# Optimization experiments

Measured on AMD Instinct MI355X. Metric: run time of the kernel, lower is better.

The kernel has to match this reference:

```python
import jax, jax.numpy as jnp
import numpy as np

T, B, D, H = 1024, 64, 512, 512


def setup_inputs() -> dict:
    key = jax.random.key(0)
    ks = jax.random.split(key, 10)
    s_in = 1.0 / np.sqrt(D + H)  # torch Linear default init scale
    inp = {
        "inputs": jax.random.normal(ks[0], (T, B, D), dtype=jnp.float32),
        "Wf": jax.random.uniform(ks[1], (D + H, H), jnp.float32, -s_in, s_in),
        "bf": jax.random.uniform(ks[2], (H,), jnp.float32, -s_in, s_in),
        "Wi": jax.random.uniform(ks[3], (D + H, H), jnp.float32, -s_in, s_in),
        "bi": jax.random.uniform(ks[4], (H,), jnp.float32, -s_in, s_in),
        "Wg": jax.random.uniform(ks[5], (D + H, H), jnp.float32, -s_in, s_in),
        "bg": jax.random.uniform(ks[6], (H,), jnp.float32, -s_in, s_in),
        "Wo": jax.random.uniform(ks[7], (D + H, H), jnp.float32, -s_in, s_in),
        "bo": jax.random.uniform(ks[8], (H,), jnp.float32, -s_in, s_in),
        "phase_bias": jax.random.normal(ks[9], (H,), dtype=jnp.float32) * 0.02,
    }
    return inp


def reference(inputs, Wf, bf, Wi, bi, Wg, bg, Wo, bo, phase_bias):
    gate_scale = 1.0
    Bsz = inputs.shape[1]
    Hd = Wf.shape[1]
    # Fuse the four gate projections into one GEMM per step (same math).
    W = jnp.concatenate([Wf, Wi, Wg, Wo], axis=1)          # [D+H, 4H]
    bias = jnp.concatenate([bf, bi, bg, bo]) * gate_scale + jnp.tile(phase_bias, 4)
    # note: (x@W + b)*s + pb == x@(W*s) + (b*s + pb); gate_scale folded in.
    Ws = W * gate_scale

    h0 = jnp.zeros((Bsz, Hd), dtype=inputs.dtype)
    c0 = jnp.zeros((Bsz, Hd), dtype=inputs.dtype)

    def step(carry, x):
        hx, cx = carry
        combined = jnp.concatenate([x, hx], axis=1)         # [B, D+H]
        z = combined @ Ws + bias                            # [B, 4H]
        zf, zi, zg, zo = jnp.split(z, 4, axis=1)
        f = jax.nn.sigmoid(zf)
        i = jax.nn.sigmoid(zi)
        g = jnp.tanh(zg)
        o = jax.nn.sigmoid(zo)
        cx = f * cx + i * g
        hx = o * jnp.tanh(cx)
        return (hx, cx), hx

    (hx, cx), stacked = jax.lax.scan(step, (h0, c0), inputs)
    return stacked, hx, cx
```

## Files before the change

kernel.cpp:

```cpp
#include <hip/hip_runtime.h>

#define TT 1024
#define BB 64
#define DD 512
#define HH 512
#define NG 4
#define BPG 16
#define NS 32
#define NTHR 256

typedef short s8v __attribute__((ext_vector_type(8)));
typedef float f4v __attribute__((ext_vector_type(4)));
typedef int i4v __attribute__((ext_vector_type(4)));

#define LGKM_BAR()                                          \
  do {                                                      \
    asm volatile("s_waitcnt lgkmcnt(0)" ::: "memory");      \
    __builtin_amdgcn_sched_barrier(0);                      \
    __builtin_amdgcn_s_barrier();                           \
    __builtin_amdgcn_sched_barrier(0);                      \
  } while (0)

static __device__ __forceinline__ unsigned short f2bf(float f) {
  union { float f; unsigned int u; } v; v.f = f;
  unsigned int r = v.u + 0x7FFFu + ((v.u >> 16) & 1u);
  return (unsigned short)(r >> 16);
}
static __device__ __forceinline__ i4v ld_b128_cohere(const void* p) {
  i4v r;
  asm volatile("global_load_dwordx4 %0, %1, off sc0 sc1"
               : "=v"(r) : "v"(p) : "memory");
  return r;
}
static __device__ __forceinline__ int ld_b32_cohere(const void* p) {
  int r;
  asm volatile("global_load_dword %0, %1, off sc0 sc1\n\t"
               "s_waitcnt vmcnt(0)"
               : "=v"(r) : "v"(p) : "memory");
  return r;
}
static __device__ __forceinline__ void st_b32_cohere(void* p, unsigned int v) {
  asm volatile("global_store_dword %0, %1, off sc0 sc1"
               :: "v"(p), "v"(v) : "memory");
}
static __device__ __forceinline__ unsigned int cvtpk_bf16(float lo, float hi) {
  unsigned int r;
  asm("v_cvt_pk_bf16_f32 %0, %1, %2" : "=v"(r) : "v"(lo), "v"(hi));
  return r;
}

__global__ void __launch_bounds__(128, 1) qlstm_init(int* flags) {
  st_b32_cohere(flags + threadIdx.x, 0u);
}

__global__ void __launch_bounds__(NTHR, 1) qlstm_main(
    const float* __restrict__ X,
    const float* __restrict__ Wf, const float* __restrict__ bfp,
    const float* __restrict__ Wi, const float* __restrict__ bip,
    const float* __restrict__ Wg, const float* __restrict__ bgp,
    const float* __restrict__ Wo, const float* __restrict__ bop,
    const float* __restrict__ phase,
    float* __restrict__ out, int* __restrict__ flags,
    unsigned short* __restrict__ hbuf) {
  __shared__ float zx[2][2][4][64][4];
  __shared__ float zh[2][4][64][4];
  const int tid   = threadIdx.x;
  const int wv    = tid >> 6;
  const int lane  = tid & 63;
  const int n     = lane & 15;
  const int kg    = lane >> 4;
  const int group = blockIdx.x & (NG - 1);
  const int slice = blockIdx.x >> 2;
  const int b0 = group * BPG;
  const int u0 = slice * 16;
  const bool isH = (wv >= 2);
  const int kh = wv & 1;

  const int wcol = u0 + (n & 7);
  s8v wreg[4][8];
#pragma unroll
  for (int T = 0; T < 4; ++T) {
    const float* Wsel = (T & 1) ? ((n < 8) ? Wg : Wo) : ((n < 8) ? Wf : Wi);
    const float* Wp = Wsel + (size_t)((isH ? 512 : 0) + kh * 256 + kg * 8) * HH
                    + wcol + (T >> 1) * 8;
#pragma unroll
    for (int kc = 0; kc < 8; ++kc)
#pragma unroll
      for (int j = 0; j < 8; ++j)
        wreg[T][kc][j] = (short)f2bf(Wp[(size_t)(kc * 32 + j) * HH]);
  }

  const int gb = tid >> 4, gu = tid & 15;
  const int uu = u0 + gu;
  const float bzf = bfp[uu] + phase[uu];
  const float bzi = bip[uu] + phase[uu];
  const float bzg = bgp[uu] + phase[uu];
  const float bzo = bop[uu] + phase[uu];
  float cst = 0.f;

  for (int p = tid; p < 2 * 4 * 64 * 4; p += NTHR) ((float*)zh)[p] = 0.f;
  float4 xv[16];
  s8v xf[8];
  if (!isH) {
    const float* Xr = X + ((size_t)0 * BB + b0 + n) * DD + kh * 256 + kg * 8;
#pragma unroll
    for (int kc = 0; kc < 8; ++kc) {
      xv[2 * kc]     = *(const float4*)(Xr + kc * 32);
      xv[2 * kc + 1] = *(const float4*)(Xr + kc * 32 + 4);
    }
#pragma unroll
    for (int kc = 0; kc < 8; ++kc) {
      union { s8v s; unsigned int d[4]; } af;
      af.d[0] = cvtpk_bf16(xv[2 * kc].x, xv[2 * kc].y);
      af.d[1] = cvtpk_bf16(xv[2 * kc].z, xv[2 * kc].w);
      af.d[2] = cvtpk_bf16(xv[2 * kc + 1].x, xv[2 * kc + 1].y);
      af.d[3] = cvtpk_bf16(xv[2 * kc + 1].z, xv[2 * kc + 1].w);
      xf[kc] = af.s;
    }
    f4v acc[4] = {{0.f,0.f,0.f,0.f},{0.f,0.f,0.f,0.f},{0.f,0.f,0.f,0.f},{0.f,0.f,0.f,0.f}};
#pragma unroll
    for (int kc = 0; kc < 8; ++kc)
#pragma unroll
      for (int T = 0; T < 4; ++T)
        acc[T] = __builtin_amdgcn_mfma_f32_16x16x32_bf16(xf[kc], wreg[T][kc], acc[T], 0, 0, 0);
#pragma unroll
    for (int T = 0; T < 4; ++T) *(f4v*)&zx[0][kh][T][lane][0] = acc[T];
    const float* X1 = X + ((size_t)1 * BB + b0 + n) * DD + kh * 256 + kg * 8;
#pragma unroll
    for (int kc = 0; kc < 8; ++kc) {
      xv[2 * kc]     = *(const float4*)(X1 + kc * 32);
      xv[2 * kc + 1] = *(const float4*)(X1 + kc * 32 + 4);
    }
  }

  int* myflag = flags + group * NS + slice;
  const int* pollp = flags + group * NS + (lane & 31);

  for (int t = 0; t < TT; ++t) {
    if (!isH) {
      if (t + 1 < TT) {
#pragma unroll
        for (int kc = 0; kc < 8; ++kc) {
          union { s8v s; unsigned int d[4]; } af;
          af.d[0] = cvtpk_bf16(xv[2 * kc].x, xv[2 * kc].y);
          af.d[1] = cvtpk_bf16(xv[2 * kc].z, xv[2 * kc].w);
          af.d[2] = cvtpk_bf16(xv[2 * kc + 1].x, xv[2 * kc + 1].y);
          af.d[3] = cvtpk_bf16(xv[2 * kc + 1].z, xv[2 * kc + 1].w);
          xf[kc] = af.s;
        }
        f4v acc[4] = {{0.f,0.f,0.f,0.f},{0.f,0.f,0.f,0.f},{0.f,0.f,0.f,0.f},{0.f,0.f,0.f,0.f}};
#pragma unroll
        for (int kc = 0; kc < 8; ++kc)
#pragma unroll
          for (int T = 0; T < 4; ++T)
            acc[T] = __builtin_amdgcn_mfma_f32_16x16x32_bf16(xf[kc], wreg[T][kc], acc[T], 0, 0, 0);
#pragma unroll
        for (int T = 0; T < 4; ++T)
          *(f4v*)&zx[(t + 1) & 1][kh][T][lane][0] = acc[T];
      }
    } else if (t > 0) {
      for (;;) {
        const int v = ld_b32_cohere(pollp);
        if (__all(v >= t)) break;
        __builtin_amdgcn_s_sleep(1);
      }
      const unsigned short* hb = hbuf + (size_t)((t - 1) & 1) * BB * HH +
                                 (size_t)(b0 + n) * HH + kh * 256 + kg * 8;
      i4v hf[8];
#pragma unroll
      for (int kc = 0; kc < 8; ++kc) hf[kc] = ld_b128_cohere(hb + kc * 32);
      asm volatile("s_waitcnt vmcnt(0)" ::: "memory");
      __builtin_amdgcn_sched_barrier(0);
      f4v acc[4] = {{0.f,0.f,0.f,0.f},{0.f,0.f,0.f,0.f},{0.f,0.f,0.f,0.f},{0.f,0.f,0.f,0.f}};
#pragma unroll
      for (int kc = 0; kc < 8; ++kc) {
        union { i4v i; s8v s; } af; af.i = hf[kc];
#pragma unroll
        for (int T = 0; T < 4; ++T)
          acc[T] = __builtin_amdgcn_mfma_f32_16x16x32_bf16(af.s, wreg[T][kc], acc[T], 0, 0, 0);
      }
#pragma unroll
      for (int T = 0; T < 4; ++T) *(f4v*)&zh[kh][T][lane][0] = acc[T];
    }
    LGKM_BAR();

    const int par = t & 1;
    const int Lf  = (gb >> 2) * 16 + (gu & 7);
    const int T0  = (gu >> 3) * 2;
    const int ci  = gb & 3;
    const float zfv = zx[par][0][T0][Lf][ci]     + zx[par][1][T0][Lf][ci]
                    + zh[0][T0][Lf][ci]          + zh[1][T0][Lf][ci] + bzf;
    const float ziv = zx[par][0][T0][Lf+8][ci]   + zx[par][1][T0][Lf+8][ci]
                    + zh[0][T0][Lf+8][ci]        + zh[1][T0][Lf+8][ci] + bzi;
    const float zgv = zx[par][0][T0+1][Lf][ci]   + zx[par][1][T0+1][Lf][ci]
                    + zh[0][T0+1][Lf][ci]        + zh[1][T0+1][Lf][ci] + bzg;
    const float zov = zx[par][0][T0+1][Lf+8][ci] + zx[par][1][T0+1][Lf+8][ci]
                    + zh[0][T0+1][Lf+8][ci]      + zh[1][T0+1][Lf+8][ci] + bzo;
    const float fg = 1.f / (1.f + __expf(-zfv));
    const float ig = 1.f / (1.f + __expf(-ziv));
    const float gg = 1.f - 2.f / (__expf(2.f * zgv) + 1.f);
    const float og = 1.f / (1.f + __expf(-zov));
    cst = fg * cst + ig * gg;
    const float hv = og * (1.f - 2.f / (__expf(2.f * cst) + 1.f));

    const float hn = __shfl_down(hv, 1);
    if (!(gu & 1))
      st_b32_cohere(hbuf + (size_t)par * BB * HH + (size_t)(b0 + gb) * HH + uu,
                    cvtpk_bf16(hv, hn));
    if (!isH && t + 2 < TT) {
      const float* Xr = X + ((size_t)(t + 2) * BB + b0 + n) * DD + kh * 256 + kg * 8;
#pragma unroll
      for (int kc = 0; kc < 8; ++kc) {
        xv[2 * kc]     = *(const float4*)(Xr + kc * 32);
        xv[2 * kc + 1] = *(const float4*)(Xr + kc * 32 + 4);
      }
      asm volatile("s_waitcnt vmcnt(16)" ::: "memory");
    } else {
      asm volatile("s_waitcnt vmcnt(0)" ::: "memory");
    }
    __builtin_amdgcn_sched_barrier(0);
    __builtin_amdgcn_s_barrier();
    __builtin_amdgcn_sched_barrier(0);
    if (tid == 0) st_b32_cohere(myflag, (unsigned int)(t + 1));

    out[(size_t)t * BB * HH + (size_t)(b0 + gb) * HH + uu] = hv;
    if (t == TT - 1) {
      out[(size_t)TT * BB * HH + (size_t)(b0 + gb) * HH + uu] = hv;
      out[(size_t)TT * BB * HH + BB * HH + (size_t)(b0 + gb) * HH + uu] = cst;
    }
    LGKM_BAR();
  }
}

extern "C" void kernel_launch(void* const* d_in, const int* in_sizes, int n_in,
                              void* d_out, int out_size, void* d_ws,
                              size_t ws_size, hipStream_t stream) {
  const float* X   = (const float*)d_in[0];
  const float* Wf  = (const float*)d_in[1];
  const float* bfp = (const float*)d_in[2];
  const float* Wi  = (const float*)d_in[3];
  const float* bip = (const float*)d_in[4];
  const float* Wg  = (const float*)d_in[5];
  const float* bgp = (const float*)d_in[6];
  const float* Wo  = (const float*)d_in[7];
  const float* bop = (const float*)d_in[8];
  const float* ph  = (const float*)d_in[9];
  float* out = (float*)d_out;

  int* flags = (int*)d_ws;
  unsigned short* hbuf = (unsigned short*)((char*)d_ws + 4096);

  qlstm_init<<<1, 128, 0, stream>>>(flags);
  qlstm_main<<<NG * NS, NTHR, 0, stream>>>(X, Wf, bfp, Wi, bip, Wg, bgp, Wo,
                                           bop, ph, out, flags, hbuf);
}
```

Before: 2.921 ms.

## Halve slices per batch group with 512-thread blocks covering 32 hidden units

Each block now handles 32 hidden units using eight waves, two column halves each split into x and h waves. Blocks per batch group drop from 32 to 16, so each step's cross-block flag poll waits on half as many producers. The grid shrinks from 128 to 64 blocks, which lowers parallelism across CUs and doubles shared-memory staging and barrier width per block.

```diff
diff --git a/kernel.cpp b/kernel.cpp
--- a/kernel.cpp
+++ b/kernel.cpp
@@ -6,8 +6,8 @@
 #define HH 512
 #define NG 4
 #define BPG 16
-#define NS 32
-#define NTHR 256
+#define NS 16
+#define NTHR 512
 
 typedef short s8v __attribute__((ext_vector_type(8)));
 typedef float f4v __attribute__((ext_vector_type(4)));
@@ -49,7 +49,7 @@
   return r;
 }
 
-__global__ void __launch_bounds__(128, 1) qlstm_init(int* flags) {
+__global__ void __launch_bounds__(64, 1) qlstm_init(int* flags) {
   st_b32_cohere(flags + threadIdx.x, 0u);
 }
 
@@ -62,8 +62,8 @@
     const float* __restrict__ phase,
     float* __restrict__ out, int* __restrict__ flags,
     unsigned short* __restrict__ hbuf) {
-  __shared__ float zx[2][2][4][64][4];
-  __shared__ float zh[2][4][64][4];
+  __shared__ float zx[2][2][2][4][64][4];
+  __shared__ float zh[2][2][4][64][4];
   const int tid   = threadIdx.x;
   const int wv    = tid >> 6;
   const int lane  = tid & 63;
@@ -72,17 +72,17 @@
   const int group = blockIdx.x & (NG - 1);
   const int slice = blockIdx.x >> 2;
   const int b0 = group * BPG;
-  const int u0 = slice * 16;
-  const bool isH = (wv >= 2);
+  const int u0 = slice * 32;
+  const bool isH = (wv >= 4);
   const int kh = wv & 1;
-
-  const int wcol = u0 + (n & 7);
+  const int ch = (wv >> 1) & 1;
+
   s8v wreg[4][8];
 #pragma unroll
   for (int T = 0; T < 4; ++T) {
     const float* Wsel = (T & 1) ? ((n < 8) ? Wg : Wo) : ((n < 8) ? Wf : Wi);
     const float* Wp = Wsel + (size_t)((isH ? 512 : 0) + kh * 256 + kg * 8) * HH
-                    + wcol + (T >> 1) * 8;
+                    + u0 + ch * 16 + (T >> 1) * 8 + (n & 7);
 #pragma unroll
     for (int kc = 0; kc < 8; ++kc)
 #pragma unroll
@@ -90,7 +90,7 @@
         wreg[T][kc][j] = (short)f2bf(Wp[(size_t)(kc * 32 + j) * HH]);
   }
 
-  const int gb = tid >> 4, gu = tid & 15;
+  const int gb = tid >> 5, gu = tid & 31;
   const int uu = u0 + gu;
   const float bzf = bfp[uu] + phase[uu];
   const float bzi = bip[uu] + phase[uu];
@@ -98,7 +98,7 @@
   const float bzo = bop[uu] + phase[uu];
   float cst = 0.f;
 
-  for (int p = tid; p < 2 * 4 * 64 * 4; p += NTHR) ((float*)zh)[p] = 0.f;
+  for (int p = tid; p < 2 * 2 * 4 * 64 * 4; p += NTHR) ((float*)zh)[p] = 0.f;
   float4 xv[16];
   s8v xf[8];
   if (!isH) {
@@ -124,7 +124,7 @@
       for (int T = 0; T < 4; ++T)
         acc[T] = __builtin_amdgcn_mfma_f32_16x16x32_bf16(xf[kc], wreg[T][kc], acc[T], 0, 0, 0);
 #pragma unroll
-    for (int T = 0; T < 4; ++T) *(f4v*)&zx[0][kh][T][lane][0] = acc[T];
+    for (int T = 0; T < 4; ++T) *(f4v*)&zx[0][kh][ch][T][lane][0] = acc[T];
     const float* X1 = X + ((size_t)1 * BB + b0 + n) * DD + kh * 256 + kg * 8;
 #pragma unroll
     for (int kc = 0; kc < 8; ++kc) {
@@ -134,7 +134,7 @@
   }
 
   int* myflag = flags + group * NS + slice;
-  const int* pollp = flags + group * NS + (lane & 31);
+  const int* pollp = flags + group * NS + (lane & 15);
 
   for (int t = 0; t < TT; ++t) {
     if (!isH) {
@@ -156,7 +156,7 @@
             acc[T] = __builtin_amdgcn_mfma_f32_16x16x32_bf16(xf[kc], wreg[T][kc], acc[T], 0, 0, 0);
 #pragma unroll
         for (int T = 0; T < 4; ++T)
-          *(f4v*)&zx[(t + 1) & 1][kh][T][lane][0] = acc[T];
+          *(f4v*)&zx[(t + 1) & 1][kh][ch][T][lane][0] = acc[T];
       }
     } else if (t > 0) {
       for (;;) {
@@ -180,22 +180,24 @@
           acc[T] = __builtin_amdgcn_mfma_f32_16x16x32_bf16(af.s, wreg[T][kc], acc[T], 0, 0, 0);
       }
 #pragma unroll
-      for (int T = 0; T < 4; ++T) *(f4v*)&zh[kh][T][lane][0] = acc[T];
+      for (int T = 0; T < 4; ++T) *(f4v*)&zh[kh][ch][T][lane][0] = acc[T];
     }
     LGKM_BAR();
 
     const int par = t & 1;
-    const int Lf  = (gb >> 2) * 16 + (gu & 7);
-    const int T0  = (gu >> 3) * 2;
+    const int cu2 = gu >> 4;
+    const int sub = gu & 15;
+    const int T0  = (sub >> 3) * 2;
+    const int Lf  = (gb >> 2) * 16 + (sub & 7);
     const int ci  = gb & 3;
-    const float zfv = zx[par][0][T0][Lf][ci]     + zx[par][1][T0][Lf][ci]
-                    + zh[0][T0][Lf][ci]          + zh[1][T0][Lf][ci] + bzf;
-    const float ziv = zx[par][0][T0][Lf+8][ci]   + zx[par][1][T0][Lf+8][ci]
-                    + zh[0][T0][Lf+8][ci]        + zh[1][T0][Lf+8][ci] + bzi;
-    const float zgv = zx[par][0][T0+1][Lf][ci]   + zx[par][1][T0+1][Lf][ci]
-                    + zh[0][T0+1][Lf][ci]        + zh[1][T0+1][Lf][ci] + bzg;
-    const float zov = zx[par][0][T0+1][Lf+8][ci] + zx[par][1][T0+1][Lf+8][ci]
-                    + zh[0][T0+1][Lf+8][ci]      + zh[1][T0+1][Lf+8][ci] + bzo;
+    const float zfv = zx[par][0][cu2][T0][Lf][ci]     + zx[par][1][cu2][T0][Lf][ci]
+                    + zh[0][cu2][T0][Lf][ci]          + zh[1][cu2][T0][Lf][ci] + bzf;
+    const float ziv = zx[par][0][cu2][T0][Lf+8][ci]   + zx[par][1][cu2][T0][Lf+8][ci]
+                    + zh[0][cu2][T0][Lf+8][ci]        + zh[1][cu2][T0][Lf+8][ci] + bzi;
+    const float zgv = zx[par][0][cu2][T0+1][Lf][ci]   + zx[par][1][cu2][T0+1][Lf][ci]
+                    + zh[0][cu2][T0+1][Lf][ci]        + zh[1][cu2][T0+1][Lf][ci] + bzg;
+    const float zov = zx[par][0][cu2][T0+1][Lf+8][ci] + zx[par][1][cu2][T0+1][Lf+8][ci]
+                    + zh[0][cu2][T0+1][Lf+8][ci]      + zh[1][cu2][T0+1][Lf+8][ci] + bzo;
     const float fg = 1.f / (1.f + __expf(-zfv));
     const float ig = 1.f / (1.f + __expf(-ziv));
     const float gg = 1.f - 2.f / (__expf(2.f * zgv) + 1.f);
@@ -250,7 +252,7 @@
   int* flags = (int*)d_ws;
   unsigned short* hbuf = (unsigned short*)((char*)d_ws + 4096);
 
-  qlstm_init<<<1, 128, 0, stream>>>(flags);
+  qlstm_init<<<1, 64, 0, stream>>>(flags);
   qlstm_main<<<NG * NS, NTHR, 0, stream>>>(X, Wf, bfp, Wi, bip, Wg, bgp, Wo,
                                            bop, ph, out, flags, hbuf);
 }
```

Result: slower. 5.505 ms (+88.5%).
